# Kernel tuning notes

Measured on AMD Instinct MI355X. Metric: run time of the kernel, lower is better.

Reference implementation:

```python
import jax, jax.numpy as jnp
import numpy as np

N, D, K = 65536, 64, 128   # points, feature dim, n_clusters
BETA = 0.0                 # distance weighting exponent offset
EPS = 1e-8


def pairwise_distance(a, b):
    # euclidean distance matrix [n, k]
    d2 = jnp.sum(a * a, 1)[:, None] + jnp.sum(b * b, 1)[None, :] - 2.0 * (a @ b.T)
    return jnp.sqrt(jnp.maximum(d2, 0.0))


def approx_cluster_filling(dist, beta):
    # differentiable soft cluster filling: inverse-distance weights with exponent (1+beta),
    # normalized per point, averaged over points -> [K]
    w = (dist + EPS) ** (-(1.0 + beta))
    w = w / jnp.sum(w, axis=1, keepdims=True)
    return jnp.mean(w, axis=0)


def wasserstein_distance(a, b):
    # sort-based per-feature 1D Wasserstein-1 distance, averaged over features
    return jnp.mean(jnp.abs(jnp.sort(a, axis=0) - jnp.sort(b, axis=0)))


def setup_inputs():
    key = jax.random.key(0)
    k1, k2, k3 = jax.random.split(key, 3)
    x = jax.random.normal(k1, (N, D), jnp.float32)
    target = jax.random.normal(k2, (N, D), jnp.float32)
    cluster_centers = jax.random.normal(k3, (K, D), jnp.float32)
    # precomputed target-side cluster statistics (LossKMeans.__init__, detached)
    dist_t = pairwise_distance(target, cluster_centers)
    prediction_target = jnp.argmin(dist_t, axis=1).astype(jnp.int32)
    filling_target = approx_cluster_filling(dist_t, BETA)
    return {"x": x, "target": target, "cluster_centers": cluster_centers,
            "prediction_target": prediction_target, "filling_target": filling_target}


def reference(x, target, cluster_centers, prediction_target, filling_target):
    # cluster-filling MSE (differentiable soft assignment)
    dist_x = pairwise_distance(x, cluster_centers)
    loss_fil = jnp.mean((approx_cluster_filling(dist_x, BETA) - filling_target) ** 2)
    # hard (detached) cluster assignment of x; concrete in eager mode
    pred_x = np.asarray(jnp.argmin(dist_x, axis=1))
    pred_t = np.asarray(prediction_target)
    loss_med = jnp.zeros((), jnp.float32)
    for c in np.unique(pred_x):  # data-dependent loop over occupied clusters (<= K)
        ix = np.nonzero(pred_x == c)[0]
        it = np.nonzero(pred_t == c)[0]
        m = min(ix.size, it.size)
        if m == 0:
            continue  # no matching target members -> skip (empty slices)
        loss_med = loss_med + wasserstein_distance(x[ix[:m]], target[it[:m]])
    return loss_fil + loss_med
```

## Files before the change

### kernel.cpp

```cpp
#include <hip/hip_runtime.h>
#include <math.h>

#define N_PTS 65536
#define DIM   64
#define K_CL  128
#define EPSV  1e-8f
#define CAP   8192


__global__ __launch_bounds__(256) void k_init(
    float* __restrict__ fill_acc, float* __restrict__ sumw,
    unsigned long long* __restrict__ pred_enc) {
  const int i = blockIdx.x * 256 + threadIdx.x;
  if (i < K_CL) fill_acc[i] = 0.0f;
  sumw[i] = 0.0f;
  pred_enc[i] = 0xFFFFFFFFFFFFFFFFull;
}

__global__ __launch_bounds__(256) void k_dist1(
    const float* __restrict__ x, const float* __restrict__ centers,
    float* __restrict__ sumw, unsigned long long* __restrict__ pred_enc,
    float* __restrict__ w)
{
  __shared__ float csq[32];
  const int kb    = blockIdx.x & 3;
  const int pb    = blockIdx.x >> 2;
  const int jbase = kb << 5;
  const int tid   = threadIdx.x;
  const int p     = pb * 256 + tid;

  if (tid < 32) {
    const float* cp = centers + (jbase + tid) * DIM;
    float s = 0.0f;
    #pragma unroll 8
    for (int d = 0; d < DIM; ++d) { float v = cp[d]; s += v * v; }
    csq[tid] = s;
  }

  float xr[DIM];
  const float4* xp = reinterpret_cast<const float4*>(x + (size_t)p * DIM);
  #pragma unroll
  for (int q = 0; q < DIM / 4; ++q) {
    float4 v = xp[q];
    xr[4 * q + 0] = v.x; xr[4 * q + 1] = v.y;
    xr[4 * q + 2] = v.z; xr[4 * q + 3] = v.w;
  }
  float xsq = 0.0f;
  #pragma unroll
  for (int d = 0; d < DIM; ++d) xsq += xr[d] * xr[d];
  __syncthreads();

  float sw = 0.0f, best = INFINITY;
  int   bj = jbase;
  #pragma unroll 2
  for (int jj = 0; jj < 32; ++jj) {
    const int j = jbase + jj;
    const float* cp = centers + j * DIM;
    float d0 = 0.f, d1 = 0.f, d2a = 0.f, d3 = 0.f;
    #pragma unroll
    for (int d = 0; d < DIM; d += 4) {
      d0  += xr[d + 0] * cp[d + 0];
      d1  += xr[d + 1] * cp[d + 1];
      d2a += xr[d + 2] * cp[d + 2];
      d3  += xr[d + 3] * cp[d + 3];
    }
    float dot  = (d0 + d1) + (d2a + d3);
    float dsq  = xsq + csq[jj] - 2.0f * dot;
    float dist = sqrtf(fmaxf(dsq, 0.0f));
    float ww   = 1.0f / (dist + EPSV);
    w[(size_t)j * N_PTS + p] = ww;
    sw += ww;
    if (dist < best) { best = dist; bj = j; }
  }
  atomicAdd(&sumw[p], sw);
  const unsigned long long enc =
      ((unsigned long long)__float_as_uint(best) << 32) | (unsigned int)bj;
  atomicMin(&pred_enc[p], enc);
}

__global__ __launch_bounds__(256) void k_pred(
    const unsigned long long* __restrict__ pred_enc,
    const float* __restrict__ sumw,
    int* __restrict__ pred_x, float* __restrict__ inv_sumw) {
  const int p = blockIdx.x * 256 + threadIdx.x;
  pred_x[p]   = (int)(pred_enc[p] & 0xFFFFFFFFull);
  inv_sumw[p] = 1.0f / sumw[p];
}

__global__ __launch_bounds__(256) void k_fill(
    const float* __restrict__ w, const float* __restrict__ inv_sumw,
    float* __restrict__ fill_acc)
{
  __shared__ float red[4];
  const int j    = blockIdx.x >> 3;
  const int seg  = blockIdx.x & 7;
  const int tid  = threadIdx.x;
  const float4* wj = reinterpret_cast<const float4*>(
      w + (size_t)j * N_PTS + seg * 8192);
  const float4* iv = reinterpret_cast<const float4*>(inv_sumw + seg * 8192);
  float s = 0.0f;
  #pragma unroll
  for (int q = 0; q < 8; ++q) {
    const int e = q * 256 + tid;
    float4 a = wj[e];
    float4 b = iv[e];
    s += a.x * b.x + a.y * b.y + a.z * b.z + a.w * b.w;
  }
  #pragma unroll
  for (int off = 32; off > 0; off >>= 1) s += __shfl_down(s, off);
  if ((tid & 63) == 0) red[tid >> 6] = s;
  __syncthreads();
  if (tid == 0)
    atomicAdd(&fill_acc[j], red[0] + red[1] + red[2] + red[3]);
}

__global__ __launch_bounds__(1024) void k_scatter(
    const int* __restrict__ pred_x, const int* __restrict__ pred_t,
    int* __restrict__ idx_x, int* __restrict__ idx_t,
    int* __restrict__ count_x, int* __restrict__ count_t)
{
  const int c    = blockIdx.x >> 1;
  const int side = blockIdx.x & 1;
  const int* __restrict__ pred = side ? pred_t : pred_x;
  int* __restrict__ out = side ? idx_t : idx_x;
  int* __restrict__ cnt = side ? count_t : count_x;

  __shared__ int wsum[16];
  const int tid = threadIdx.x, lane = tid & 63, w = tid >> 6;
  const int beg = w * 4096;

  int cw = 0;
  for (int s = 0; s < 4096; s += 64) {
    const bool m = (pred[beg + s + lane] == c);
    cw += __popcll(__ballot(m));
  }
  if (lane == 0) wsum[w] = cw;
  __syncthreads();
  int base = 0, tot = 0;
  #pragma unroll
  for (int k = 0; k < 16; ++k) { int v = wsum[k]; tot += v; if (k < w) base += v; }

  int run = base;
  for (int s = 0; s < 4096; s += 64) {
    const int i = beg + s + lane;
    const bool m = (pred[i] == c);
    unsigned long long bal = __ballot(m);
    int lp = __popcll(bal & ((1ull << lane) - 1ull));
    if (m) { int pos = run + lp; if (pos < CAP) out[c * CAP + pos] = i; }
    run += __popcll(bal);
  }
  if (tid == 0) cnt[c] = tot;
}

__global__ __launch_bounds__(128) void k_offsets(
    const int* __restrict__ count_x, const int* __restrict__ count_t,
    int* __restrict__ offc, int* __restrict__ ord)
{
  __shared__ int sm[128];
  __shared__ int mm[128];
  const int tid = threadIdx.x;
  const int m  = min(min(count_x[tid], CAP), min(count_t[tid], CAP));
  const int sz = ((m + 3) & ~3) * DIM;
  sm[tid] = sz;
  mm[tid] = m;
  __syncthreads();
  int rank = 0;
  for (int j = 0; j < 128; ++j) {
    const int mj = mm[j];
    if (mj > m || (mj == m && j < tid)) ++rank;
  }
  ord[rank] = tid;
  for (int s = 1; s < 128; s <<= 1) {
    int v = (tid >= s) ? sm[tid - s] : 0;
    __syncthreads();
    sm[tid] += v;
    __syncthreads();
  }
  offc[tid] = sm[tid] - sz;
}

__device__ __forceinline__ void ce(float& a, float& b, bool up) {
  float lo = fminf(a, b), hi = fmaxf(a, b);
  a = up ? lo : hi;
  b = up ? hi : lo;
}

__device__ __forceinline__ void merge8(float* v, bool up) {
  ce(v[0],v[4],up); ce(v[1],v[5],up); ce(v[2],v[6],up); ce(v[3],v[7],up);
  ce(v[0],v[2],up); ce(v[1],v[3],up); ce(v[4],v[6],up); ce(v[5],v[7],up);
  ce(v[0],v[1],up); ce(v[2],v[3],up); ce(v[4],v[5],up); ce(v[6],v[7],up);
}

__device__ __forceinline__ void sort8(float* v, bool up8) {
  ce(v[0],v[1],true );  ce(v[2],v[3],false); ce(v[4],v[5],true );  ce(v[6],v[7],false);
  ce(v[0],v[2],true );  ce(v[1],v[3],true );  ce(v[4],v[6],false); ce(v[5],v[7],false);
  ce(v[0],v[1],true );  ce(v[2],v[3],true );  ce(v[4],v[5],false); ce(v[6],v[7],false);
  merge8(v, up8);
}

__device__ __forceinline__ void merge16(float* v, bool up) {
  #pragma unroll
  for (int e = 0; e < 8; ++e) ce(v[e], v[e + 8], up);
  merge8(v, up);
  merge8(v + 8, up);
}

__device__ __forceinline__ void sort16(float* v, bool up16) {
  sort8(v, true);
  sort8(v + 8, false);
  merge16(v, up16);
}

__device__ __forceinline__ void stage_one8(float v[8], int ib, int k, bool up) {
  for (int j = (k >> 1) > 256 ? 256 : (k >> 1); j >= 8; j >>= 1) {
    const int  jl = j >> 3;
    const bool tm = (up == ((ib & j) == 0));
    float p[8];
    #pragma unroll
    for (int e = 0; e < 8; ++e) p[e] = __shfl_xor(v[e], jl, 64);
    if (tm) {
      #pragma unroll
      for (int e = 0; e < 8; ++e) v[e] = fminf(v[e], p[e]);
    } else {
      #pragma unroll
      for (int e = 0; e < 8; ++e) v[e] = fmaxf(v[e], p[e]);
    }
  }
  merge8(v, up);
}

__device__ __forceinline__ void stage_one16(float v[16], int ib, int k, bool up) {
  #pragma unroll
  for (int j = (k >> 1) > 512 ? 512 : (k >> 1); j >= 16; j >>= 1) {
    const int  jl = j >> 4;
    const bool tm = (up == ((ib & j) == 0));
    float p[16];
    #pragma unroll
    for (int e = 0; e < 16; ++e) p[e] = __shfl_xor(v[e], jl, 64);
    if (tm) {
      #pragma unroll
      for (int e = 0; e < 16; ++e) v[e] = fminf(v[e], p[e]);
    } else {
      #pragma unroll
      for (int e = 0; e < 16; ++e) v[e] = fmaxf(v[e], p[e]);
    }
  }
  merge16(v, up);
}

__device__ __forceinline__ void gather8(const float* __restrict__ src,
                                        const int* __restrict__ idxc,
                                        int d, int ib, int m, float v[8]) {
  #pragma unroll
  for (int e = 0; e < 8; ++e) {
    const int r = ib + e;
    v[e] = (r < m) ? src[(size_t)idxc[r] * DIM + d] : INFINITY;
  }
}

__device__ __forceinline__ void gather16(const float* __restrict__ src,
                                         const int* __restrict__ idxc,
                                         int d, int ib, int m, float v[16]) {
  #pragma unroll
  for (int e = 0; e < 16; ++e) {
    const int r = ib + e;
    v[e] = (r < m) ? src[(size_t)idxc[r] * DIM + d] : INFINITY;
  }
}

__device__ __forceinline__ int swz4(int fi) {
  return fi ^ (((fi >> 5) & 7) << 2);
}

template<int P>
__device__ __forceinline__ void sort_col(float v[16], int ib, bool act,
                                         const float* __restrict__ src,
                                         const int* __restrict__ idxc,
                                         int d, int m, float* __restrict__ sa) {
  if (act) {
    gather16(src, idxc, d, ib, m, v);
    sort16(v, ((ib & 16) == 0));
    #pragma unroll
    for (int k = 32; k <= 1024; k <<= 1)
      stage_one16(v, ib, k, ((ib & k) == 0));
  }
  #pragma unroll
  for (int k = 2048; k <= P; k <<= 1) {
    const bool up = ((ib & k) == 0);
    #pragma unroll
    for (int j = k >> 1; j >= 1024; j >>= 1) {
      __syncthreads();
      if (act) {
        #pragma unroll
        for (int q = 0; q < 4; ++q)
          *(float4*)&sa[swz4(ib + 4*q)] =
              make_float4(v[4*q], v[4*q+1], v[4*q+2], v[4*q+3]);
      }
      __syncthreads();
      if (act) {
        const int pi = ib ^ j;
        const bool tm = (up == ((ib & j) == 0));
        float A[16];
        #pragma unroll
        for (int q = 0; q < 4; ++q) {
          float4 f = *(const float4*)&sa[swz4(pi + 4*q)];
          A[4*q+0]=f.x; A[4*q+1]=f.y; A[4*q+2]=f.z; A[4*q+3]=f.w;
        }
        if (tm) {
          #pragma unroll
          for (int e = 0; e < 16; ++e) v[e] = fminf(v[e], A[e]);
        } else {
          #pragma unroll
          for (int e = 0; e < 16; ++e) v[e] = fmaxf(v[e], A[e]);
        }
      }
    }
    if (act) stage_one16(v, ib, k, up);
  }
}

template<int P>
__device__ __forceinline__ void sort_col_io(const float* __restrict__ src,
                                            const int* __restrict__ idxc,
                                            int d, float* __restrict__ col,
                                            int m, int mp, int tid,
                                            float* __restrict__ sa) {
  const int ib = tid << 4;
  const bool act = (ib < P);
  float v[16];
  sort_col<P>(v, ib, act, src, idxc, d, m, sa);
  if (act) {
    #pragma unroll
    for (int q = 0; q < 4; ++q)
      if (ib + 4 * q < mp)
        *(float4*)&col[ib + 4*q] =
            make_float4(v[4*q], v[4*q+1], v[4*q+2], v[4*q+3]);
  }
}

__global__ __launch_bounds__(512) void k_sort(
    const float* __restrict__ x, const float* __restrict__ t,
    const int* __restrict__ idx_x, const int* __restrict__ idx_t,
    float* __restrict__ gxT, float* __restrict__ gtT,
    const int* __restrict__ offc,
    const int* __restrict__ count_x, const int* __restrict__ count_t,
    const int* __restrict__ ord)
{
  __shared__ float sa[8192];
  const int tid = threadIdx.x;

  if (blockIdx.x < 16384) {
    const int side = blockIdx.x >> 13;
    const int cd   = blockIdx.x & 8191;
    const int c = ord[cd >> 6], d = cd & 63;
    const int m = min(min(count_x[c], CAP), min(count_t[c], CAP));
    if (m <= 1024) return;
    const int mp = (m + 3) & ~3;
    const float* src  = side ? t : x;
    const int*   idxc = (side ? idx_t : idx_x) + c * CAP;
    float* col = (side ? gtT : gxT) + offc[c] + (size_t)d * mp;
    if (m <= 2048)      sort_col_io<2048>(src, idxc, d, col, m, mp, tid, sa);
    else if (m <= 4096) sort_col_io<4096>(src, idxc, d, col, m, mp, tid, sa);
    else                sort_col_io<8192>(src, idxc, d, col, m, mp, tid, sa);
  } else {
    const int base = (blockIdx.x - 16384) * 8 + (tid >> 6);
    const int lane = tid & 63;
    const int side = base >> 13;
    const int cd   = base & 8191;
    const int c = ord[cd >> 6], d = cd & 63;
    const int m = min(min(count_x[c], CAP), min(count_t[c], CAP));
    if (m > 1024 || m == 0) return;
    const int mp = (m + 3) & ~3;
    const float* src  = side ? t : x;
    const int*   idxc = (side ? idx_t : idx_x) + c * CAP;
    float* col = (side ? gtT : gxT) + offc[c] + (size_t)d * mp;

    if (m <= 512) {
      int P = 8;
      while (P < m) P <<= 1;
      const int ib = lane << 3;
      float v[8];
      gather8(src, idxc, d, ib, m, v);
      sort8(v, ((ib & 8) == 0));
      for (int k = 16; k <= P; k <<= 1)
        stage_one8(v, ib, k, ((ib & k) == 0));
      #pragma unroll
      for (int q = 0; q < 2; ++q)
        if (ib + 4 * q < mp)
          *(float4*)&col[ib + 4*q] =
              make_float4(v[4*q], v[4*q+1], v[4*q+2], v[4*q+3]);
    } else {
      const int ib = lane << 4;
      float v[16];
      gather16(src, idxc, d, ib, m, v);
      sort16(v, ((ib & 16) == 0));
      #pragma unroll
      for (int k = 32; k <= 1024; k <<= 1)
        stage_one16(v, ib, k, ((ib & k) == 0));
      #pragma unroll
      for (int q = 0; q < 4; ++q)
        if (ib + 4 * q < mp)
          *(float4*)&col[ib + 4*q] =
              make_float4(v[4*q], v[4*q+1], v[4*q+2], v[4*q+3]);
    }
  }
}

__global__ __launch_bounds__(256) void k_diff(
    const float* __restrict__ gxT, const float* __restrict__ gtT,
    const int* __restrict__ offc,
    const int* __restrict__ count_x, const int* __restrict__ count_t,
    float* __restrict__ parts)
{
  __shared__ float red[4];
  const int task = blockIdx.x;
  const int c = task >> 6, d = task & 63;
  const int m = min(min(count_x[c], CAP), min(count_t[c], CAP));
  const int tid = threadIdx.x;
  if (m == 0) { if (tid == 0) parts[task] = 0.0f; return; }
  const int mp = (m + 3) & ~3;
  const float* colx = gxT + offc[c] + (size_t)d * mp;
  const float* colt = gtT + offc[c] + (size_t)d * mp;
  float s = 0.0f;
  for (int r = tid * 4; r < mp; r += 1024) {
    float4 a = *(const float4*)&colx[r];
    float4 b = *(const float4*)&colt[r];
    if (r + 3 < m) {
      s += fabsf(a.x-b.x) + fabsf(a.y-b.y) + fabsf(a.z-b.z) + fabsf(a.w-b.w);
    } else {
      if (r + 0 < m) s += fabsf(a.x - b.x);
      if (r + 1 < m) s += fabsf(a.y - b.y);
      if (r + 2 < m) s += fabsf(a.z - b.z);
      if (r + 3 < m) s += fabsf(a.w - b.w);
    }
  }
  #pragma unroll
  for (int off = 32; off > 0; off >>= 1) s += __shfl_down(s, off);
  if ((tid & 63) == 0) red[tid >> 6] = s;
  __syncthreads();
  if (tid == 0)
    parts[task] = (red[0] + red[1] + red[2] + red[3]) / (float)(m * DIM);
}

__global__ __launch_bounds__(1024) void k_final(
    const float* __restrict__ fill_acc, const float* __restrict__ ft,
    const float* __restrict__ parts, float* __restrict__ out)
{
  __shared__ float red[16];
  const int tid = threadIdx.x;
  float s = 0.0f;
  #pragma unroll
  for (int i = 0; i < 8; ++i) s += parts[tid + i * 1024];
  if (tid < K_CL) {
    float v = fill_acc[tid] * (1.0f / (float)N_PTS) - ft[tid];
    s += v * v * (1.0f / (float)K_CL);
  }
  #pragma unroll
  for (int off = 32; off > 0; off >>= 1) s += __shfl_down(s, off);
  if ((tid & 63) == 0) red[tid >> 6] = s;
  __syncthreads();
  if (tid == 0) {
    float tot = 0.0f;
    #pragma unroll
    for (int w = 0; w < 16; ++w) tot += red[w];
    out[0] = tot;
  }
}

extern "C" void kernel_launch(void* const* d_in, const int* in_sizes, int n_in,
                              void* d_out, int out_size, void* d_ws, size_t ws_size,
                              hipStream_t stream)
{
  (void)in_sizes; (void)n_in; (void)out_size; (void)ws_size;
  const float* x      = (const float*)d_in[0];
  const float* target = (const float*)d_in[1];
  const float* cc     = (const float*)d_in[2];
  const int*   pred_t = (const int*)d_in[3];
  const float* ft     = (const float*)d_in[4];
  float* out = (float*)d_out;

  char* ws = (char*)d_ws;
  float* fill_acc = (float*)(ws + 0);
  int*   pred_x   = (int*)(ws + 1024);
  int*   idx_x    = (int*)(ws + 263168);
  int*   idx_t    = (int*)(ws + 4457472);
  int*   count_x  = (int*)(ws + 8651776);
  int*   count_t  = (int*)(ws + 8651776 + 512);
  float* parts    = (float*)(ws + 8652800);
  float* sumw     = (float*)(ws + 8685568);
  float* inv_sumw = (float*)(ws + 8947712);
  unsigned long long* pred_enc = (unsigned long long*)(ws + 9209856);
  int*   offc     = (int*)(ws + 9734144);
  int*   ord      = (int*)(ws + 9734656);
  float* gxT      = (float*)(ws + 9735168);
  float* gtT      = (float*)(ws + 26643456);
  float* wmat     = (float*)(ws + 9735168);

  k_init<<<N_PTS / 256, 256, 0, stream>>>(fill_acc, sumw, pred_enc);
  k_dist1<<<N_PTS / 256 * 4, 256, 0, stream>>>(x, cc, sumw, pred_enc, wmat);
  k_pred<<<N_PTS / 256, 256, 0, stream>>>(pred_enc, sumw, pred_x, inv_sumw);
  k_fill<<<K_CL * 8, 256, 0, stream>>>(wmat, inv_sumw, fill_acc);
  k_scatter<<<K_CL * 2, 1024, 0, stream>>>(pred_x, pred_t, idx_x, idx_t,
                                           count_x, count_t);
  k_offsets<<<1, 128, 0, stream>>>(count_x, count_t, offc, ord);
  k_sort<<<16384 + 2048, 512, 0, stream>>>(x, target, idx_x, idx_t,
                                           gxT, gtT, offc,
                                           count_x, count_t, ord);
  k_diff<<<K_CL * DIM, 256, 0, stream>>>(gxT, gtT, offc,
                                         count_x, count_t, parts);
  k_final<<<1, 1024, 0, stream>>>(fill_acc, ft, parts, out);
}
```

Measured before the change: 284.1 us.

## Balance sort blocks across XCD slots with greedy cluster-to-slot assignment

Replaces the sorted cluster order with two slot maps built in k_offsets. Large clusters go greedily to 8 slots by estimated m·log²m cost, and small clusters are assigned round-robin. k_sort derives its cluster from blockIdx&7 so that consecutive blocks, which hardware schedules round-robin across the 8 XCDs, carry balanced work. This targets load imbalance between chiplets in the sort kernel. The cost is a serial single-thread loop in k_offsets, and the maps reuse workspace memory that pred_enc used earlier.

```diff
diff --git a/kernel.cpp b/kernel.cpp
--- a/kernel.cpp
+++ b/kernel.cpp
@@ -154,22 +154,53 @@
 
 __global__ __launch_bounds__(128) void k_offsets(
     const int* __restrict__ count_x, const int* __restrict__ count_t,
-    int* __restrict__ offc, int* __restrict__ ord)
+    int* __restrict__ offc, int* __restrict__ ls_map, int* __restrict__ tl_map)
 {
   __shared__ int sm[128];
   __shared__ int mm[128];
+  __shared__ int ords[128];
   const int tid = threadIdx.x;
   const int m  = min(min(count_x[tid], CAP), min(count_t[tid], CAP));
   const int sz = ((m + 3) & ~3) * DIM;
   sm[tid] = sz;
   mm[tid] = m;
+  ls_map[tid] = -1;
+  tl_map[tid] = -1;
   __syncthreads();
   int rank = 0;
   for (int j = 0; j < 128; ++j) {
     const int mj = mm[j];
     if (mj > m || (mj == m && j < tid)) ++rank;
   }
-  ord[rank] = tid;
+  ords[rank] = tid;
+  __syncthreads();
+  if (tid == 0) {
+    long long load[8];
+    int cnt[8], tcnt[8];
+    #pragma unroll
+    for (int s = 0; s < 8; ++s) { load[s] = 0; cnt[s] = 0; tcnt[s] = 0; }
+    int tpos = 0;
+    for (int r = 0; r < 128; ++r) {
+      const int c  = ords[r];
+      const int mc = mm[c];
+      if (mc > 1024) {
+        int best = -1;
+        #pragma unroll
+        for (int s = 0; s < 8; ++s)
+          if (cnt[s] < 16 && (best < 0 || load[s] < load[best])) best = s;
+        const int lg = 32 - __clz(mc - 1);
+        ls_map[best * 16 + cnt[best]] = c;
+        cnt[best]++;
+        load[best] += (long long)mc * lg * lg;
+      } else if (mc > 0) {
+        const int s = tpos & 7;
+        tl_map[s * 16 + tcnt[s]] = c;
+        tcnt[s]++;
+        ++tpos;
+      }
+    }
+  }
+  __syncthreads();
   for (int s = 1; s < 128; s <<= 1) {
     int v = (tid >= s) ? sm[tid - s] : 0;
     __syncthreads();
@@ -344,15 +375,20 @@
     float* __restrict__ gxT, float* __restrict__ gtT,
     const int* __restrict__ offc,
     const int* __restrict__ count_x, const int* __restrict__ count_t,
-    const int* __restrict__ ord)
+    const int* __restrict__ ls_map, const int* __restrict__ tl_map)
 {
   __shared__ float sa[8192];
   const int tid = threadIdx.x;
 
   if (blockIdx.x < 16384) {
-    const int side = blockIdx.x >> 13;
-    const int cd   = blockIdx.x & 8191;
-    const int c = ord[cd >> 6], d = cd & 63;
+    const int slot = blockIdx.x & 7;
+    const int q    = blockIdx.x >> 3;
+    const int i    = q >> 7;
+    const int task = q & 127;
+    const int c    = ls_map[slot * 16 + i];
+    if (c < 0) return;
+    const int side = task >> 6;
+    const int d    = task & 63;
     const int m = min(min(count_x[c], CAP), min(count_t[c], CAP));
     if (m <= 1024) return;
     const int mp = (m + 3) & ~3;
@@ -363,11 +399,18 @@
     else if (m <= 4096) sort_col_io<4096>(src, idxc, d, col, m, mp, tid, sa);
     else                sort_col_io<8192>(src, idxc, d, col, m, mp, tid, sa);
   } else {
-    const int base = (blockIdx.x - 16384) * 8 + (tid >> 6);
+    const int tb   = blockIdx.x - 16384;
+    const int slot = tb & 7;
+    const int q    = tb >> 3;
+    const int j    = q >> 4;
+    const int blk16 = q & 15;
+    const int c    = tl_map[slot * 16 + j];
+    if (c < 0) return;
+    const int wv   = tid >> 6;
     const int lane = tid & 63;
-    const int side = base >> 13;
-    const int cd   = base & 8191;
-    const int c = ord[cd >> 6], d = cd & 63;
+    const int task = blk16 * 8 + wv;
+    const int side = task >> 6;
+    const int d    = task & 63;
     const int m = min(min(count_x[c], CAP), min(count_t[c], CAP));
     if (m > 1024 || m == 0) return;
     const int mp = (m + 3) & ~3;
@@ -385,10 +428,10 @@
       for (int k = 16; k <= P; k <<= 1)
         stage_one8(v, ib, k, ((ib & k) == 0));
       #pragma unroll
-      for (int q = 0; q < 2; ++q)
-        if (ib + 4 * q < mp)
-          *(float4*)&col[ib + 4*q] =
-              make_float4(v[4*q], v[4*q+1], v[4*q+2], v[4*q+3]);
+      for (int q2 = 0; q2 < 2; ++q2)
+        if (ib + 4 * q2 < mp)
+          *(float4*)&col[ib + 4*q2] =
+              make_float4(v[4*q2], v[4*q2+1], v[4*q2+2], v[4*q2+3]);
     } else {
       const int ib = lane << 4;
       float v[16];
@@ -398,10 +441,10 @@
       for (int k = 32; k <= 1024; k <<= 1)
         stage_one16(v, ib, k, ((ib & k) == 0));
       #pragma unroll
-      for (int q = 0; q < 4; ++q)
-        if (ib + 4 * q < mp)
-          *(float4*)&col[ib + 4*q] =
-              make_float4(v[4*q], v[4*q+1], v[4*q+2], v[4*q+3]);
+      for (int q2 = 0; q2 < 4; ++q2)
+        if (ib + 4 * q2 < mp)
+          *(float4*)&col[ib + 4*q2] =
+              make_float4(v[4*q2], v[4*q2+1], v[4*q2+2], v[4*q2+3]);
     }
   }
 }
@@ -490,8 +533,9 @@
   float* sumw     = (float*)(ws + 8685568);
   float* inv_sumw = (float*)(ws + 8947712);
   unsigned long long* pred_enc = (unsigned long long*)(ws + 9209856);
+  int*   ls_map   = (int*)(ws + 9209856);
+  int*   tl_map   = (int*)(ws + 9210368);
   int*   offc     = (int*)(ws + 9734144);
-  int*   ord      = (int*)(ws + 9734656);
   float* gxT      = (float*)(ws + 9735168);
   float* gtT      = (float*)(ws + 26643456);
   float* wmat     = (float*)(ws + 9735168);
@@ -502,10 +546,10 @@
   k_fill<<<K_CL * 8, 256, 0, stream>>>(wmat, inv_sumw, fill_acc);
   k_scatter<<<K_CL * 2, 1024, 0, stream>>>(pred_x, pred_t, idx_x, idx_t,
                                            count_x, count_t);
-  k_offsets<<<1, 128, 0, stream>>>(count_x, count_t, offc, ord);
+  k_offsets<<<1, 128, 0, stream>>>(count_x, count_t, offc, ls_map, tl_map);
   k_sort<<<16384 + 2048, 512, 0, stream>>>(x, target, idx_x, idx_t,
                                            gxT, gtT, offc,
-                                           count_x, count_t, ord);
+                                           count_x, count_t, ls_map, tl_map);
   k_diff<<<K_CL * DIM, 256, 0, stream>>>(gxT, gtT, offc,
                                          count_x, count_t, parts);
   k_final<<<1, 1024, 0, stream>>>(fill_acc, ft, parts, out);
```

Result: slower. 303.1 us (+6.7%).
